# Kernel optimization log

Hardware: AMD Instinct MI355X
Metric: run time of the kernel (lower is better)

The kernel has to match this reference:

```python
import jax, jax.numpy as jnp
import numpy as np

B, S, H = 64, 2048, 512


def setup_inputs() -> dict:
    key = jax.random.key(0)
    ks = jax.random.split(key, 11)
    sc = 1.0 / np.sqrt(H)
    return {
        "encoder_output": jax.random.normal(ks[0], (B, S, H), jnp.float32),
        "decoder_hidden": jax.random.normal(ks[1], (B, H), jnp.float32),
        "coverage": jax.random.uniform(ks[2], (B, S), jnp.float32),
        # params (torch Linear: y = x @ W.T + b); we store W already transposed as [in, out]
        "Wh": jax.random.normal(ks[3], (H, H), jnp.float32) * sc,
        "bh": jax.random.normal(ks[4], (H,), jnp.float32) * sc,
        "Ws": jax.random.normal(ks[5], (H, H), jnp.float32) * sc,
        "bs": jax.random.normal(ks[6], (H,), jnp.float32) * sc,
        "Wc": jax.random.normal(ks[7], (1, H), jnp.float32) * sc,  # Linear(1, H)
        "bc": jax.random.normal(ks[8], (H,), jnp.float32) * sc,
        "v_w": jax.random.normal(ks[9], (H,), jnp.float32) * sc,   # Linear(H, 1) weight
        "v_b": jax.random.normal(ks[10], (1,), jnp.float32) * sc,
    }


def reference(encoder_output, decoder_hidden, coverage, Wh, bh, Ws, bs, Wc, bc, v_w, v_b):
    # encoder_feature: [B,S,H]
    enc_f = jnp.einsum('bsh,hk->bsk', encoder_output, Wh) + bh
    # decoder_feature: [B,1,H]
    dec_f = (decoder_hidden @ Ws + bs)[:, None, :]
    # coverage_feature: [B,S,H] = cov[...,None] @ Wc(1,H) + bc
    cov_f = coverage[:, :, None] * Wc[0] + bc
    feat = jnp.tanh(enc_f + dec_f + cov_f)          # [B,S,H]
    e_t = jnp.einsum('bsh,h->bs', feat, v_w) + v_b[0]  # [B,S]
    a_t = jax.nn.softmax(e_t, axis=-1)
    sum_coverage = coverage + a_t
    return a_t, sum_coverage
```

## Files before the change

### kernel.cpp

```cpp
#include <hip/hip_runtime.h>
#include <math.h>


#define B_ 64
#define S_ 2048
#define H_ 512
#define M_ (B_ * S_)

#define RPB 128
#define BN 16
#define NPH 32
#define PHS (BN * H_)
#define PHBYTES (PHS * 2)

typedef __attribute__((ext_vector_type(4))) float f32x4;
typedef __attribute__((ext_vector_type(8))) short s16x8;
typedef unsigned int u32;

__device__ __forceinline__ short f2bf(float f) {
    unsigned u = __float_as_uint(f);
    u += 0x7fffu + ((u >> 16) & 1u);
    return (short)(u >> 16);
}

__device__ __forceinline__ s16x8 cvt8(float4 a, float4 b) {
    s16x8 r;
    r[0] = f2bf(a.x); r[1] = f2bf(a.y); r[2] = f2bf(a.z); r[3] = f2bf(a.w);
    r[4] = f2bf(b.x); r[5] = f2bf(b.y); r[6] = f2bf(b.z); r[7] = f2bf(b.w);
    return r;
}

__device__ __forceinline__ float fast_tanh(float x) {
    return 1.0f - 2.0f / (__expf(2.0f * x) + 1.0f);
}

__device__ __forceinline__ void dma16(const void* g, void* s) {
    __builtin_amdgcn_global_load_lds(
        (const __attribute__((address_space(1))) u32*)g,
        (__attribute__((address_space(3))) u32*)s, 16, 0, 0);
}

__global__ __launch_bounds__(256) void transpose_cast(
    const float* __restrict__ Wh, short* __restrict__ Bimg) {
    __shared__ float tile[32][33];
    const int n0 = blockIdx.x * 32, k0 = blockIdx.y * 32;
    const int tx = threadIdx.x & 31, ty = threadIdx.x >> 5;
#pragma unroll
    for (int r = 0; r < 32; r += 8)
        tile[ty + r][tx] = Wh[(size_t)(k0 + ty + r) * H_ + n0 + tx];
    __syncthreads();
    const int kw = k0 >> 5;
    const int q = tx >> 3, j = tx & 7;
#pragma unroll
    for (int r = 0; r < 32; r += 8) {
        const int n = n0 + ty + r;
        const int ph = n >> 4, mln = n & 15;
        const size_t idx = (size_t)ph * PHS + (size_t)kw * 512
                         + q * 128 + mln * 8 + j;
        Bimg[idx] = f2bf(tile[tx][ty + r]);
    }
}

__global__ __launch_bounds__(256) void dec_kernel(
    const float* __restrict__ dh, const float* __restrict__ Ws,
    const float* __restrict__ bs, const float* __restrict__ bh,
    const float* __restrict__ bc, float* __restrict__ D) {
    const int b = blockIdx.x;
    const int h = blockIdx.y * 256 + threadIdx.x;
    __shared__ float sdh[H_];
    sdh[threadIdx.x] = dh[b * H_ + threadIdx.x];
    sdh[threadIdx.x + 256] = dh[b * H_ + threadIdx.x + 256];
    __syncthreads();
    float acc = bs[h] + bh[h] + bc[h];
#pragma unroll 8
    for (int k = 0; k < H_; ++k)
        acc = fmaf(sdh[k], Ws[k * H_ + h], acc);
    D[b * H_ + h] = acc;
}

__global__ __launch_bounds__(256, 3) void gemm_fused(
    const float* __restrict__ A,
    const short* __restrict__ Bimg,
    const float* __restrict__ cover,
    const float* __restrict__ Wc,
    const float* __restrict__ vw,
    const float* __restrict__ D,
    float* __restrict__ e_t) {
    __shared__ __align__(16) short Bs[3 * PHS];

    const int tid = threadIdx.x;
    const int w = tid >> 6;
    const int l = tid & 63;
    const int q = l >> 4;
    const int ml = l & 15;

    const int row_blk = blockIdx.x * RPB;
    const int b = row_blk >> 11;
    const int r0 = row_blk + w * 32;

    const int chunk0 = w * 4;

    {
        const char* g0 = (const char*)Bimg + chunk0 * 1024 + l * 16;
        char* s0 = (char*)Bs + chunk0 * 1024;
#pragma unroll
        for (int c = 0; c < 4; ++c) dma16(g0 + c * 1024, s0 + c * 1024);
        const char* g1 = g0 + PHBYTES;
        char* s1 = s0 + PHBYTES;
#pragma unroll
        for (int c = 0; c < 4; ++c) dma16(g1 + c * 1024, s1 + c * 1024);
    }

    s16x8 a[2][16];
    {
        const float* ap = A + (size_t)(r0 + ml) * H_ + q * 8;
#pragma unroll
        for (int kw = 0; kw < 16; ++kw) {
#pragma unroll
            for (int t = 0; t < 2; ++t) {
                const float* p = ap + (size_t)t * 16 * H_ + kw * 32;
                float4 x = *(const float4*)p;
                float4 y = *(const float4*)(p + 4);
                a[t][kw] = cvt8(x, y);
            }
        }
    }

    float cv[2][4];
#pragma unroll
    for (int t = 0; t < 2; ++t)
#pragma unroll
        for (int r = 0; r < 4; ++r)
            cv[t][r] = cover[r0 + t * 16 + q * 4 + r];

    float ecur[2][4] = {};

    int cur = 0;
    const char* gdma = (const char*)Bimg + 2 * (size_t)PHBYTES
                     + chunk0 * 1024 + l * 16;

    for (int p = 0; p < NPH; ++p) {
        asm volatile("s_waitcnt vmcnt(4)" ::: "memory");
        __builtin_amdgcn_sched_barrier(0);
        __builtin_amdgcn_s_barrier();

        const int n0 = p * BN + ml;
        const float wc = Wc[n0];
        const float vv = vw[n0];
        const float dd = D[b * H_ + n0];
        __builtin_amdgcn_sched_barrier(0);

        if (p + 2 < NPH) {
            const int nb = (cur == 0) ? 2 : cur - 1;
            char* sd = (char*)Bs + nb * PHBYTES + chunk0 * 1024;
#pragma unroll
            for (int c = 0; c < 4; ++c) dma16(gdma + c * 1024, sd + c * 1024);
            gdma += PHBYTES;
        }

        const short* bp = Bs + cur * PHS;
        f32x4 acc0 = (f32x4)0.0f, acc1 = (f32x4)0.0f;
#pragma unroll
        for (int kw = 0; kw < 16; ++kw) {
            s16x8 bfr = *(const s16x8*)(bp + kw * 512 + l * 8);
            acc0 = __builtin_amdgcn_mfma_f32_16x16x32_bf16(a[0][kw], bfr, acc0, 0, 0, 0);
            acc1 = __builtin_amdgcn_mfma_f32_16x16x32_bf16(a[1][kw], bfr, acc1, 0, 0, 0);
        }

#pragma unroll
        for (int r = 0; r < 4; ++r) {
            ecur[0][r] += vv * fast_tanh(acc0[r] + fmaf(cv[0][r], wc, dd));
            ecur[1][r] += vv * fast_tanh(acc1[r] + fmaf(cv[1][r], wc, dd));
        }

        cur = (cur == 2) ? 0 : cur + 1;
    }

#pragma unroll
    for (int t = 0; t < 2; ++t) {
        float p0 = ecur[t][0], p1 = ecur[t][1], p2 = ecur[t][2], p3 = ecur[t][3];
#pragma unroll
        for (int s = 1; s < 16; s <<= 1) {
            p0 += __shfl_xor(p0, s, 64);
            p1 += __shfl_xor(p1, s, 64);
            p2 += __shfl_xor(p2, s, 64);
            p3 += __shfl_xor(p3, s, 64);
        }
        if (ml == 0) {
            float4 st = {p0, p1, p2, p3};
            *(float4*)&e_t[r0 + t * 16 + q * 4] = st;
        }
    }
}

__global__ __launch_bounds__(256) void softmax_kernel(
    const float* __restrict__ e_t, const float* __restrict__ cover,
    const float* __restrict__ vb, float* __restrict__ out) {
    const int b = blockIdx.x;
    const int tid = threadIdx.x;
    const float vbv = vb[0];

    float e[8];
    float mx = -1e30f;
#pragma unroll
    for (int r = 0; r < 8; ++r) {
        e[r] = e_t[b * S_ + r * 256 + tid] + vbv;
        mx = fmaxf(mx, e[r]);
    }
#pragma unroll
    for (int off = 32; off >= 1; off >>= 1) mx = fmaxf(mx, __shfl_xor(mx, off, 64));

    __shared__ float sm[4], ss[4], sbc[2];
    const int wid = tid >> 6, lane = tid & 63;
    if (lane == 0) sm[wid] = mx;
    __syncthreads();
    if (tid == 0) sbc[0] = fmaxf(fmaxf(sm[0], sm[1]), fmaxf(sm[2], sm[3]));
    __syncthreads();
    mx = sbc[0];

    float ex[8];
    float sum = 0.0f;
#pragma unroll
    for (int r = 0; r < 8; ++r) {
        ex[r] = __expf(e[r] - mx);
        sum += ex[r];
    }
#pragma unroll
    for (int off = 32; off >= 1; off >>= 1) sum += __shfl_xor(sum, off, 64);
    if (lane == 0) ss[wid] = sum;
    __syncthreads();
    if (tid == 0) sbc[1] = ss[0] + ss[1] + ss[2] + ss[3];
    __syncthreads();
    const float inv = 1.0f / sbc[1];

#pragma unroll
    for (int r = 0; r < 8; ++r) {
        const int s = r * 256 + tid;
        const float a = ex[r] * inv;
        out[b * S_ + s] = a;
        out[M_ + b * S_ + s] = cover[b * S_ + s] + a;
    }
}

extern "C" void kernel_launch(void* const* d_in, const int* in_sizes, int n_in,
                              void* d_out, int out_size, void* d_ws, size_t ws_size,
                              hipStream_t stream) {
    const float* enc = (const float*)d_in[0];
    const float* dh  = (const float*)d_in[1];
    const float* cov = (const float*)d_in[2];
    const float* Wh  = (const float*)d_in[3];
    const float* bh  = (const float*)d_in[4];
    const float* Ws  = (const float*)d_in[5];
    const float* bs  = (const float*)d_in[6];
    const float* Wc  = (const float*)d_in[7];
    const float* bc  = (const float*)d_in[8];
    const float* vw  = (const float*)d_in[9];
    const float* vb  = (const float*)d_in[10];
    float* out = (float*)d_out;

    float* e_t  = (float*)d_ws;
    float* Dws  = e_t + M_;
    short* Whbt = (short*)(Dws + B_ * H_);

    transpose_cast<<<dim3(H_ / 32, H_ / 32), 256, 0, stream>>>(Wh, Whbt);
    dec_kernel<<<dim3(B_, 2), 256, 0, stream>>>(dh, Ws, bs, bh, bc, Dws);
    gemm_fused<<<M_ / RPB, 256, 0, stream>>>(enc, Whbt, cov, Wc, vw, Dws, e_t);
    softmax_kernel<<<B_, 256, 0, stream>>>(e_t, cov, vb, out);
}
```

Baseline: 573.4 us.

## Stream Wh fragments from global into registers instead of LDS triple-buffer

Removes the LDS triple-buffered DMA pipeline and its per-phase barriers. Each wave now loads B fragments directly from global memory (served from L2) into a rolling 8-deep register prefetch ring. Launch bounds drop from 3 to 2 blocks per CU to make room for the extra registers. The trade is no barriers or LDS use against redundant global/L2 traffic for every wave and lower occupancy.

```diff
diff --git a/kernel.cpp b/kernel.cpp
--- a/kernel.cpp
+++ b/kernel.cpp
@@ -7,15 +7,12 @@
 #define H_ 512
 #define M_ (B_ * S_)
 
-#define RPB 128
-#define BN 16
-#define NPH 32
-#define PHS (BN * H_)
-#define PHBYTES (PHS * 2)
+#define NT 32
+#define NFRAG 512
+#define FRAG_SHORTS 512
 
 typedef __attribute__((ext_vector_type(4))) float f32x4;
 typedef __attribute__((ext_vector_type(8))) short s16x8;
-typedef unsigned int u32;
 
 __device__ __forceinline__ short f2bf(float f) {
     unsigned u = __float_as_uint(f);
@@ -34,12 +31,6 @@
     return 1.0f - 2.0f / (__expf(2.0f * x) + 1.0f);
 }
 
-__device__ __forceinline__ void dma16(const void* g, void* s) {
-    __builtin_amdgcn_global_load_lds(
-        (const __attribute__((address_space(1))) u32*)g,
-        (__attribute__((address_space(3))) u32*)s, 16, 0, 0);
-}
-
 __global__ __launch_bounds__(256) void transpose_cast(
     const float* __restrict__ Wh, short* __restrict__ Bimg) {
     __shared__ float tile[32][33];
@@ -54,8 +45,8 @@
 #pragma unroll
     for (int r = 0; r < 32; r += 8) {
         const int n = n0 + ty + r;
-        const int ph = n >> 4, mln = n & 15;
-        const size_t idx = (size_t)ph * PHS + (size_t)kw * 512
+        const int nt = n >> 4, mln = n & 15;
+        const size_t idx = (size_t)nt * 8192 + (size_t)kw * FRAG_SHORTS
                          + q * 128 + mln * 8 + j;
         Bimg[idx] = f2bf(tile[tx][ty + r]);
     }
@@ -78,7 +69,7 @@
     D[b * H_ + h] = acc;
 }
 
-__global__ __launch_bounds__(256, 3) void gemm_fused(
+__global__ __launch_bounds__(256, 2) void gemm_fused(
     const float* __restrict__ A,
     const short* __restrict__ Bimg,
     const float* __restrict__ cover,
@@ -86,30 +77,21 @@
     const float* __restrict__ vw,
     const float* __restrict__ D,
     float* __restrict__ e_t) {
-    __shared__ __align__(16) short Bs[3 * PHS];
-
     const int tid = threadIdx.x;
     const int w = tid >> 6;
     const int l = tid & 63;
     const int q = l >> 4;
     const int ml = l & 15;
-
-    const int row_blk = blockIdx.x * RPB;
-    const int b = row_blk >> 11;
-    const int r0 = row_blk + w * 32;
-
-    const int chunk0 = w * 4;
-
-    {
-        const char* g0 = (const char*)Bimg + chunk0 * 1024 + l * 16;
-        char* s0 = (char*)Bs + chunk0 * 1024;
-#pragma unroll
-        for (int c = 0; c < 4; ++c) dma16(g0 + c * 1024, s0 + c * 1024);
-        const char* g1 = g0 + PHBYTES;
-        char* s1 = s0 + PHBYTES;
-#pragma unroll
-        for (int c = 0; c < 4; ++c) dma16(g1 + c * 1024, s1 + c * 1024);
-    }
+    const int l8 = l * 8;
+
+    const int wave_id = blockIdx.x * 4 + w;
+    const int r0 = wave_id * 32;
+    const int b = r0 >> 11;
+
+    s16x8 bf[8];
+#pragma unroll
+    for (int f = 0; f < 8; ++f)
+        bf[f] = *(const s16x8*)(Bimg + (size_t)f * FRAG_SHORTS + l8);
 
     s16x8 a[2][16];
     {
@@ -135,45 +117,29 @@
 
     float ecur[2][4] = {};
 
-    int cur = 0;
-    const char* gdma = (const char*)Bimg + 2 * (size_t)PHBYTES
-                     + chunk0 * 1024 + l * 16;
-
-    for (int p = 0; p < NPH; ++p) {
-        asm volatile("s_waitcnt vmcnt(4)" ::: "memory");
-        __builtin_amdgcn_sched_barrier(0);
-        __builtin_amdgcn_s_barrier();
-
-        const int n0 = p * BN + ml;
-        const float wc = Wc[n0];
-        const float vv = vw[n0];
-        const float dd = D[b * H_ + n0];
-        __builtin_amdgcn_sched_barrier(0);
-
-        if (p + 2 < NPH) {
-            const int nb = (cur == 0) ? 2 : cur - 1;
-            char* sd = (char*)Bs + nb * PHBYTES + chunk0 * 1024;
-#pragma unroll
-            for (int c = 0; c < 4; ++c) dma16(gdma + c * 1024, sd + c * 1024);
-            gdma += PHBYTES;
-        }
-
-        const short* bp = Bs + cur * PHS;
+#pragma unroll 1
+    for (int nt = 0; nt < NT; ++nt) {
+        const int n0 = nt * 16 + ml;
+        const float wcv = Wc[n0];
+        const float vvv = vw[n0];
+        const float ddv = D[b * H_ + n0];
+
         f32x4 acc0 = (f32x4)0.0f, acc1 = (f32x4)0.0f;
 #pragma unroll
         for (int kw = 0; kw < 16; ++kw) {
-            s16x8 bfr = *(const s16x8*)(bp + kw * 512 + l * 8);
-            acc0 = __builtin_amdgcn_mfma_f32_16x16x32_bf16(a[0][kw], bfr, acc0, 0, 0, 0);
-            acc1 = __builtin_amdgcn_mfma_f32_16x16x32_bf16(a[1][kw], bfr, acc1, 0, 0, 0);
+            const s16x8 cur = bf[kw & 7];
+            int fn = nt * 16 + kw + 8;
+            if (fn > NFRAG - 1) fn = NFRAG - 1;
+            bf[kw & 7] = *(const s16x8*)(Bimg + (size_t)fn * FRAG_SHORTS + l8);
+            acc0 = __builtin_amdgcn_mfma_f32_16x16x32_bf16(a[0][kw], cur, acc0, 0, 0, 0);
+            acc1 = __builtin_amdgcn_mfma_f32_16x16x32_bf16(a[1][kw], cur, acc1, 0, 0, 0);
         }
 
 #pragma unroll
         for (int r = 0; r < 4; ++r) {
-            ecur[0][r] += vv * fast_tanh(acc0[r] + fmaf(cv[0][r], wc, dd));
-            ecur[1][r] += vv * fast_tanh(acc1[r] + fmaf(cv[1][r], wc, dd));
-        }
-
-        cur = (cur == 2) ? 0 : cur + 1;
+            ecur[0][r] += vvv * fast_tanh(acc0[r] + fmaf(cv[0][r], wcv, ddv));
+            ecur[1][r] += vvv * fast_tanh(acc1[r] + fmaf(cv[1][r], wcv, ddv));
+        }
     }
 
 #pragma unroll
@@ -264,6 +230,6 @@
 
     transpose_cast<<<dim3(H_ / 32, H_ / 32), 256, 0, stream>>>(Wh, Whbt);
     dec_kernel<<<dim3(B_, 2), 256, 0, stream>>>(dh, Ws, bs, bh, bc, Dws);
-    gemm_fused<<<M_ / RPB, 256, 0, stream>>>(enc, Whbt, cov, Wc, vw, Dws, e_t);
+    gemm_fused<<<M_ / 128, 256, 0, stream>>>(enc, Whbt, cov, Wc, vw, Dws, e_t);
     softmax_kernel<<<B_, 256, 0, stream>>>(e_t, cov, vb, out);
 }
```

New measurement: 500.2 us. 12.8% less time.
